# Kernel optimization log

Hardware: AMD Instinct MI355X
Metric: run time of the kernel (lower is better)

Reference implementation:

```python
import math
import jax, jax.numpy as jnp
import numpy as np

B, S, DIM = 1, 2048, 2048
N_HEADS, N_KV_HEADS = 32, 8
HEAD_DIM = DIM // N_HEADS  # 64
HIDDEN = 8192  # 4*dim, already a multiple of 256
EPS = 1e-5


def setup_inputs() -> dict:
    key = jax.random.key(0)
    ks = jax.random.split(key, 10)

    def xavier(k, shape):
        lim = math.sqrt(6.0 / (shape[0] + shape[1]))
        return jax.random.uniform(k, shape, jnp.float32, -lim, lim)

    x = jax.random.normal(ks[0], (B, S, DIM), jnp.float32)
    c = jax.random.normal(ks[1], (B, DIM), jnp.float32)
    x_mask = jnp.ones((B, S), dtype=bool)
    # RoPE angles (theta=10000), freqs_cis = exp(i * pos * inv_freq) -> cos/sin parts
    inv_freq = 1.0 / (10000.0 ** (jnp.arange(0, HEAD_DIM, 2, dtype=jnp.float32) / HEAD_DIM))
    ang = jnp.arange(S, dtype=jnp.float32)[:, None] * inv_freq[None, :]  # [S, HEAD_DIM//2]
    freqs_cos = jnp.broadcast_to(jnp.cos(ang)[None], (B, S, HEAD_DIM // 2))
    freqs_sin = jnp.broadcast_to(jnp.sin(ang)[None], (B, S, HEAD_DIM // 2))
    qkv_out = (N_HEADS + 2 * N_KV_HEADS) * HEAD_DIM
    return dict(
        x=x, x_mask=x_mask, freqs_cos=freqs_cos, freqs_sin=freqs_sin, c=c,
        w_qkv=xavier(ks[2], (qkv_out, DIM)),
        w_out=xavier(ks[3], (DIM, N_HEADS * HEAD_DIM)),
        q_norm_w=jnp.ones((HEAD_DIM,), jnp.float32),
        k_norm_w=jnp.ones((HEAD_DIM,), jnp.float32),
        attn_norm1_w=jnp.ones((DIM,), jnp.float32),
        attn_norm2_w=jnp.ones((DIM,), jnp.float32),
        ffn_norm1_w=jnp.ones((DIM,), jnp.float32),
        ffn_norm2_w=jnp.ones((DIM,), jnp.float32),
        w1=xavier(ks[4], (HIDDEN, DIM)),
        w2=xavier(ks[5], (DIM, HIDDEN)),
        w3=xavier(ks[6], (HIDDEN, DIM)),
        w_ada=0.02 * jax.random.normal(ks[7], (4 * DIM, DIM), jnp.float32),
        b_ada=jnp.zeros((4 * DIM,), jnp.float32),
    )


def rms_norm(x, w, eps=EPS):
    x32 = x.astype(jnp.float32)
    return (x32 * jax.lax.rsqrt(jnp.mean(x32 * x32, -1, keepdims=True) + eps)).astype(x.dtype) * w


def apply_rope(x, cos, sin):
    # x: [b,s,h,d]; complex pairing of consecutive elements (view_as_complex)
    xr, xi = x[..., 0::2], x[..., 1::2]
    c = cos[:, :, None, :]  # broadcast over heads (freqs_cis.unsqueeze(2))
    s = sin[:, :, None, :]
    return jnp.stack([xr * c - xi * s, xr * s + xi * c], axis=-1).reshape(x.shape)


def reference(x, x_mask, freqs_cos, freqs_sin, c, w_qkv, w_out, q_norm_w, k_norm_w,
              attn_norm1_w, attn_norm2_w, ffn_norm1_w, ffn_norm2_w, w1, w2, w3,
              w_ada, b_ada):
    b, s, _ = x.shape
    n_rep = N_HEADS // N_KV_HEADS
    # AdaLN modulation: SiLU -> Linear -> 4 chunks
    mod = jax.nn.silu(c) @ w_ada.T + b_ada                      # [b, 4*dim]
    scale_msa, gate_msa, scale_mlp, gate_mlp = jnp.split(mod, 4, axis=-1)
    # ---- attention branch ----
    h = rms_norm(x, attn_norm1_w) * (1.0 + scale_msa[:, None, :])
    qkv = h @ w_qkv.T
    q, k, v = jnp.split(qkv, [N_HEADS * HEAD_DIM, (N_HEADS + N_KV_HEADS) * HEAD_DIM], axis=-1)
    q = q.reshape(b, s, N_HEADS, HEAD_DIM)
    k = k.reshape(b, s, N_KV_HEADS, HEAD_DIM)
    v = v.reshape(b, s, N_KV_HEADS, HEAD_DIM)
    q = rms_norm(q, q_norm_w)
    k = rms_norm(k, k_norm_w)
    q = apply_rope(q, freqs_cos, freqs_sin)
    k = apply_rope(k, freqs_cos, freqs_sin)
    # GQA: repeat each kv head n_rep times consecutively (unsqueeze+repeat+flatten)
    k = jnp.repeat(k, n_rep, axis=2)
    v = jnp.repeat(v, n_rep, axis=2)
    scale = math.sqrt(1.0 / HEAD_DIM)
    scores = jnp.einsum('bqhd,bkhd->bhqk', q, k) * scale         # [b,H,s,s]
    scores = jnp.where(x_mask[:, None, None, :], scores, -1e30)
    probs = jax.nn.softmax(scores, axis=-1)
    attn = jnp.einsum('bhqk,bkhd->bqhd', probs, v).reshape(b, s, N_HEADS * HEAD_DIM)
    attn = attn @ w_out.T
    x = x + jnp.tanh(gate_msa)[:, None, :] * rms_norm(attn, attn_norm2_w)
    # ---- SwiGLU FFN branch ----
    h = rms_norm(x, ffn_norm1_w) * (1.0 + scale_mlp[:, None, :])
    ffn = (jax.nn.silu(h @ w1.T) * (h @ w3.T)) @ w2.T
    x = x + jnp.tanh(gate_mlp)[:, None, :] * rms_norm(ffn, ffn_norm2_w)
    return x
```

## Files before the change

### kernel.cpp

```cpp
#include <hip/hip_runtime.h>
#include <hip/hip_bf16.h>
#include <cstdint>

typedef __hip_bfloat16 bf16;
typedef __attribute__((ext_vector_type(8))) short s8v;
typedef __attribute__((ext_vector_type(4))) float f32x4;

#define MFMA_BF16(a,b,c) __builtin_amdgcn_mfma_f32_16x16x32_bf16((a),(b),(c),0,0,0)

__device__ __forceinline__ float bf2f(bf16 v) { return __bfloat162float(v); }
__device__ __forceinline__ bf16 f2bf(float v) { return __float2bfloat16(v); }
__device__ __forceinline__ short f2bfbits(float v) {
  bf16 b = __float2bfloat16(v);
  short s; __builtin_memcpy(&s, &b, 2); return s;
}
__device__ __forceinline__ void g2lds16(const void* g, void* l) {
  __builtin_amdgcn_global_load_lds((__attribute__((address_space(1))) void*)(g),
                                   (__attribute__((address_space(3))) void*)(l), 16, 0, 0);
}
__device__ __forceinline__ void load8(const bf16* p, float v[8]) {
  uint4 r = *reinterpret_cast<const uint4*>(p);
  v[0]=__uint_as_float(r.x<<16); v[1]=__uint_as_float(r.x&0xffff0000u);
  v[2]=__uint_as_float(r.y<<16); v[3]=__uint_as_float(r.y&0xffff0000u);
  v[4]=__uint_as_float(r.z<<16); v[5]=__uint_as_float(r.z&0xffff0000u);
  v[6]=__uint_as_float(r.w<<16); v[7]=__uint_as_float(r.w&0xffff0000u);
}
__device__ __forceinline__ void loadf8(const float* p, float v[8]) {
  float4 a = *(const float4*)p, b = *(const float4*)(p + 4);
  v[0]=a.x; v[1]=a.y; v[2]=a.z; v[3]=a.w;
  v[4]=b.x; v[5]=b.y; v[6]=b.z; v[7]=b.w;
}
__device__ __forceinline__ s8v cvt8(const float* p) {
  float4 a = *(const float4*)p, b = *(const float4*)(p + 4);
  s8v r;
  r[0]=f2bfbits(a.x); r[1]=f2bfbits(a.y); r[2]=f2bfbits(a.z); r[3]=f2bfbits(a.w);
  r[4]=f2bfbits(b.x); r[5]=f2bfbits(b.y); r[6]=f2bfbits(b.z); r[7]=f2bfbits(b.w);
  return r;
}

__global__ __launch_bounds__(256) void ndt_cvt(
    const float* __restrict__ s, bf16* __restrict__ d, long n) {
  long i = ((long)blockIdx.x * 256 + threadIdx.x) * 8;
  if (i >= n) return;
  *(s8v*)(d + i) = cvt8(s + i);
}

__global__ __launch_bounds__(256) void ndt_ada(
    const float* __restrict__ c, const float* __restrict__ w_ada,
    const float* __restrict__ b_ada, float* __restrict__ mods) {
  const int wave = threadIdx.x >> 6, lane = threadIdx.x & 63;
  const int out = blockIdx.x * 4 + wave;
  const float4* wrow = (const float4*)(w_ada + (long)out * 2048);
  const float4* c4 = (const float4*)c;
  float acc = 0.f;
  for (int k = lane; k < 512; k += 64) {
    float4 wv = wrow[k];
    float4 cv = c4[k];
    acc += (cv.x / (1.f + __expf(-cv.x))) * wv.x;
    acc += (cv.y / (1.f + __expf(-cv.y))) * wv.y;
    acc += (cv.z / (1.f + __expf(-cv.z))) * wv.z;
    acc += (cv.w / (1.f + __expf(-cv.w))) * wv.w;
  }
  #pragma unroll
  for (int o = 32; o; o >>= 1) acc += __shfl_xor(acc, o, 64);
  if (lane == 0) {
    float m = acc + b_ada[out];
    int grp = out >> 11, idx = out & 2047;
    mods[grp * 2048 + idx] = (grp & 1) ? tanhf(m) : (1.f + m);
  }
}

__global__ __launch_bounds__(256) void ndt_norm_mod(
    const float* __restrict__ x, const float* __restrict__ w,
    const float* __restrict__ smod, bf16* __restrict__ out) {
  const int t = blockIdx.x, tid = threadIdx.x;
  __shared__ float red[4];
  float v[8];
  loadf8(x + (long)t * 2048 + tid * 8, v);
  float ss = 0.f;
  #pragma unroll
  for (int i = 0; i < 8; i++) ss += v[i] * v[i];
  #pragma unroll
  for (int o = 32; o; o >>= 1) ss += __shfl_xor(ss, o, 64);
  if ((tid & 63) == 0) red[tid >> 6] = ss;
  __syncthreads();
  float r = rsqrtf((red[0]+red[1]+red[2]+red[3]) * (1.f/2048.f) + 1e-5f);
  #pragma unroll
  for (int i = 0; i < 8; i++) {
    int cc = tid * 8 + i;
    out[(long)t * 2048 + cc] = f2bf(v[i] * r * w[cc] * smod[cc]);
  }
}

template<int EPI>
__global__ __launch_bounds__(256) void ndt_gemm_bb(
    const bf16* __restrict__ A, const bf16* __restrict__ B,
    bf16* __restrict__ C, const bf16* __restrict__ aux,
    int M, int N, int K) {
  __shared__ alignas(16) short sA[128 * 32];
  __shared__ alignas(16) short sB[128 * 32];
  const int tid = threadIdx.x;
  const int wave = tid >> 6, lane = tid & 63;
  const int quad = lane >> 4, l15 = lane & 15;
  const int wm = (wave >> 1) << 6, wn = (wave & 1) << 6;
  const long m0 = (long)blockIdx.x * 128, n0 = (long)blockIdx.y * 128;
  f32x4 zero4 = {0.f, 0.f, 0.f, 0.f};
  f32x4 acc[4][4];
  #pragma unroll
  for (int i = 0; i < 4; i++)
    #pragma unroll
    for (int j = 0; j < 4; j++) acc[i][j] = zero4;
  const int srow = lane >> 2;
  const int skc  = (lane & 3) * 8;
  for (int k0 = 0; k0 < K; k0 += 32) {
    #pragma unroll
    for (int it = 0; it < 2; it++) {
      int seg = wave * 2 + it;
      int row = seg * 16 + srow;
      g2lds16(A + (m0 + row) * (long)K + k0 + skc, (char*)sA + seg * 1024);
      g2lds16(B + (n0 + row) * (long)K + k0 + skc, (char*)sB + seg * 1024);
    }
    __syncthreads();
    s8v af[4], bfr[4];
    #pragma unroll
    for (int i = 0; i < 4; i++) af[i]  = *(const s8v*)&sA[(wm + i*16 + l15)*32 + quad*8];
    #pragma unroll
    for (int j = 0; j < 4; j++) bfr[j] = *(const s8v*)&sB[(wn + j*16 + l15)*32 + quad*8];
    #pragma unroll
    for (int i = 0; i < 4; i++)
      #pragma unroll
      for (int j = 0; j < 4; j++)
        acc[i][j] = MFMA_BF16(af[i], bfr[j], acc[i][j]);
    __syncthreads();
  }
  #pragma unroll
  for (int i = 0; i < 4; i++) {
    long rg = m0 + wm + i*16 + quad*4;
    #pragma unroll
    for (int j = 0; j < 4; j++) {
      long cg = n0 + wn + j*16 + l15;
      #pragma unroll
      for (int r = 0; r < 4; r++) {
        float v = acc[i][j][r];
        long idx = (rg + r) * (long)N + cg;
        if (EPI == 1) v = v / (1.f + __expf(-v));
        if (EPI == 2) v = v * bf2f(aux[idx]);
        C[idx] = f2bf(v);
      }
    }
  }
}

template<int EPI>
__global__ __launch_bounds__(256) void ndt_gemm_bt(
    const bf16* __restrict__ A, const float* __restrict__ B,
    bf16* __restrict__ C, const bf16* __restrict__ aux,
    int M, int N, int K) {
  __shared__ alignas(16) short sA[128 * 32];
  __shared__ alignas(16) short sB[128 * 32];
  const int tid = threadIdx.x;
  const int wave = tid >> 6, lane = tid & 63;
  const int quad = lane >> 4, l15 = lane & 15;
  const int wm = (wave >> 1) << 6, wn = (wave & 1) << 6;
  const long m0 = (long)blockIdx.x * 128, n0 = (long)blockIdx.y * 128;
  f32x4 zero4 = {0.f, 0.f, 0.f, 0.f};
  f32x4 acc[4][4];
  #pragma unroll
  for (int i = 0; i < 4; i++)
    #pragma unroll
    for (int j = 0; j < 4; j++) acc[i][j] = zero4;
  const int srow = lane >> 2;
  const int skc  = (lane & 3) * 8;
  const int r0 = (wave * 2) * 16 + srow;
  const int r1 = (wave * 2 + 1) * 16 + srow;
  const bf16*  pa0 = A + (m0 + r0) * (long)K + skc;
  const bf16*  pa1 = A + (m0 + r1) * (long)K + skc;
  const float* pb0 = B + (n0 + r0) * (long)K + skc;
  const float* pb1 = B + (n0 + r1) * (long)K + skc;
  uint4* da0 = (uint4*)&sA[r0 * 32 + skc];
  uint4* da1 = (uint4*)&sA[r1 * 32 + skc];
  s8v* db0 = (s8v*)&sB[r0 * 32 + skc];
  s8v* db1 = (s8v*)&sB[r1 * 32 + skc];
  for (int k0 = 0; k0 < K; k0 += 32) {
    uint4 va0 = *(const uint4*)pa0; pa0 += 32;
    uint4 va1 = *(const uint4*)pa1; pa1 += 32;
    s8v vb0 = cvt8(pb0); pb0 += 32;
    s8v vb1 = cvt8(pb1); pb1 += 32;
    *da0 = va0; *da1 = va1; *db0 = vb0; *db1 = vb1;
    __syncthreads();
    s8v af[4], bfr[4];
    #pragma unroll
    for (int i = 0; i < 4; i++) af[i]  = *(const s8v*)&sA[(wm + i*16 + l15)*32 + quad*8];
    #pragma unroll
    for (int j = 0; j < 4; j++) bfr[j] = *(const s8v*)&sB[(wn + j*16 + l15)*32 + quad*8];
    #pragma unroll
    for (int i = 0; i < 4; i++)
      #pragma unroll
      for (int j = 0; j < 4; j++)
        acc[i][j] = MFMA_BF16(af[i], bfr[j], acc[i][j]);
    __syncthreads();
  }
  #pragma unroll
  for (int i = 0; i < 4; i++) {
    long rg = m0 + wm + i*16 + quad*4;
    #pragma unroll
    for (int j = 0; j < 4; j++) {
      long cg = n0 + wn + j*16 + l15;
      #pragma unroll
      for (int r = 0; r < 4; r++) {
        float v = acc[i][j][r];
        long idx = (rg + r) * (long)N + cg;
        if (EPI == 1) v = v / (1.f + __expf(-v));
        if (EPI == 2) v = v * bf2f(aux[idx]);
        C[idx] = f2bf(v);
      }
    }
  }
}

__global__ __launch_bounds__(256) void ndt_qkrope(
    const bf16* __restrict__ qkv, const float* __restrict__ qw, const float* __restrict__ kw,
    const float* __restrict__ fc, const float* __restrict__ fs,
    bf16* __restrict__ qb, bf16* __restrict__ kb, bf16* __restrict__ vb) {
  const int wid = blockIdx.x * 4 + (threadIdx.x >> 6);
  const int lane = threadIdx.x & 63;
  const int t = wid / 48;
  const int u = wid - t * 48;
  if (u < 40) {
    const bool isq = (u < 32);
    const int hh = isq ? u : (u - 32);
    const long src = (long)t * 3072 + (isq ? hh * 64 : 2048 + hh * 64) + lane;
    float v = bf2f(qkv[src]);
    float ss = v * v;
    #pragma unroll
    for (int o = 32; o; o >>= 1) ss += __shfl_xor(ss, o, 64);
    float r = rsqrtf(ss * (1.f/64.f) + 1e-5f);
    float y = v * r * (isq ? qw[lane] : kw[lane]);
    int j = lane >> 1;
    float cv = fc[t * 32 + j];
    float sv = fs[t * 32 + j];
    float p = __shfl_xor(y, 1, 64);
    float out = (lane & 1) ? (p * sv + y * cv) : (y * cv - p * sv);
    if (isq) qb[(long)t * 2048 + hh * 64 + lane] = f2bf(out);
    else     kb[(long)t * 512 + hh * 64 + lane] = f2bf(out);
  } else {
    const int vh = u - 40;
    vb[(long)t * 512 + vh * 64 + lane] = qkv[(long)t * 3072 + 2560 + vh * 64 + lane];
  }
}

__global__ __launch_bounds__(256) void ndt_attn(
    const bf16* __restrict__ qb, const bf16* __restrict__ kb,
    const bf16* __restrict__ vb, bf16* __restrict__ ob) {
  const int h = blockIdx.y;
  const int qblk = blockIdx.x;
  const int tid = threadIdx.x;
  const int wave = tid >> 6, lane = tid & 63;
  const int quad = lane >> 4, l15 = lane & 15;
  const int kh = h >> 2;
  __shared__ alignas(16) short kT[64 * 72];
  __shared__ alignas(16) short vT[64 * 72];
  __shared__ alignas(16) short pT[4][16 * 72];
  const int qrow = qblk * 64 + wave * 16 + l15;
  const short* qptr = (const short*)qb + (long)qrow * 2048 + h * 64;
  s8v qf0 = *(const s8v*)(qptr + quad * 8);
  s8v qf1 = *(const s8v*)(qptr + 32 + quad * 8);
  f32x4 zero4 = {0.f, 0.f, 0.f, 0.f};
  f32x4 o[4];
  float mr[4], lr[4];
  #pragma unroll
  for (int r = 0; r < 4; r++) { o[r] = zero4; mr[r] = -1e30f; lr[r] = 0.f; }
  const int skey = tid >> 2;
  const int sdg = (tid & 3) * 16;
  for (int kt = 0; kt < 32; kt++) {
    {
      const short* ksrc = (const short*)kb + ((long)(kt * 64 + skey) * 8 + kh) * 64 + sdg;
      *(uint4*)&kT[skey * 72 + sdg]     = *(const uint4*)(ksrc);
      *(uint4*)&kT[skey * 72 + sdg + 8] = *(const uint4*)(ksrc + 8);
      const short* vsrc = (const short*)vb + ((long)(kt * 64 + skey) * 8 + kh) * 64 + sdg;
      short tv[16];
      *(uint4*)&tv[0] = *(const uint4*)(vsrc);
      *(uint4*)&tv[8] = *(const uint4*)(vsrc + 8);
      #pragma unroll
      for (int i = 0; i < 16; i++) vT[(sdg + i) * 72 + skey] = tv[i];
    }
    __syncthreads();
    f32x4 s[4];
    #pragma unroll
    for (int b4 = 0; b4 < 4; b4++) {
      const short* kr = &kT[(b4 * 16 + l15) * 72];
      s8v kf0 = *(const s8v*)(kr + quad * 8);
      s8v kf1 = *(const s8v*)(kr + 32 + quad * 8);
      f32x4 z = zero4;
      z = MFMA_BF16(qf0, kf0, z);
      z = MFMA_BF16(qf1, kf1, z);
      s[b4] = z;
    }
    #pragma unroll
    for (int r = 0; r < 4; r++) {
      float mx = -1e30f;
      #pragma unroll
      for (int b4 = 0; b4 < 4; b4++) { float sv2 = s[b4][r] * 0.125f; s[b4][r] = sv2; mx = fmaxf(mx, sv2); }
      mx = fmaxf(mx, __shfl_xor(mx, 1, 64));
      mx = fmaxf(mx, __shfl_xor(mx, 2, 64));
      mx = fmaxf(mx, __shfl_xor(mx, 4, 64));
      mx = fmaxf(mx, __shfl_xor(mx, 8, 64));
      float nm = fmaxf(mr[r], mx);
      float alpha = __expf(mr[r] - nm);
      mr[r] = nm;
      float rs = 0.f;
      #pragma unroll
      for (int b4 = 0; b4 < 4; b4++) { float p = __expf(s[b4][r] - nm); s[b4][r] = p; rs += p; }
      rs += __shfl_xor(rs, 1, 64);
      rs += __shfl_xor(rs, 2, 64);
      rs += __shfl_xor(rs, 4, 64);
      rs += __shfl_xor(rs, 8, 64);
      lr[r] = lr[r] * alpha + rs;
      #pragma unroll
      for (int cb = 0; cb < 4; cb++) o[cb][r] *= alpha;
    }
    short* pw = &pT[wave][0];
    #pragma unroll
    for (int b4 = 0; b4 < 4; b4++)
      #pragma unroll
      for (int r = 0; r < 4; r++)
        pw[(quad * 4 + r) * 72 + b4 * 16 + l15] = f2bfbits(s[b4][r]);
    const short* pr = &pT[wave][0];
    s8v pf0 = *(const s8v*)(pr + l15 * 72 + quad * 8);
    s8v pf1 = *(const s8v*)(pr + l15 * 72 + 32 + quad * 8);
    #pragma unroll
    for (int cb = 0; cb < 4; cb++) {
      const short* vr = &vT[(cb * 16 + l15) * 72];
      s8v vf0 = *(const s8v*)(vr + quad * 8);
      s8v vf1 = *(const s8v*)(vr + 32 + quad * 8);
      o[cb] = MFMA_BF16(pf0, vf0, o[cb]);
      o[cb] = MFMA_BF16(pf1, vf1, o[cb]);
    }
    __syncthreads();
  }
  #pragma unroll
  for (int cb = 0; cb < 4; cb++)
    #pragma unroll
    for (int r = 0; r < 4; r++) {
      int tok = qblk * 64 + wave * 16 + quad * 4 + r;
      ob[(long)tok * 2048 + h * 64 + cb * 16 + l15] = f2bf(o[cb][r] / lr[r]);
    }
}

__global__ __launch_bounds__(256) void ndt_resid1(
    const float* __restrict__ x, const bf16* __restrict__ ao,
    const float* __restrict__ mods, const float* __restrict__ w_n2,
    const float* __restrict__ w_f1, float* __restrict__ x1, bf16* __restrict__ h2) {
  const int t = blockIdx.x, tid = threadIdx.x;
  __shared__ float red1[4], red2[4];
  const long base = (long)t * 2048;
  float a[8], xv[8], y[8];
  load8(ao + base + tid * 8, a);
  loadf8(x + base + tid * 8, xv);
  float ss = 0.f;
  #pragma unroll
  for (int i = 0; i < 8; i++) ss += a[i] * a[i];
  #pragma unroll
  for (int o = 32; o; o >>= 1) ss += __shfl_xor(ss, o, 64);
  if ((tid & 63) == 0) red1[tid >> 6] = ss;
  __syncthreads();
  float r1 = rsqrtf((red1[0]+red1[1]+red1[2]+red1[3]) * (1.f/2048.f) + 1e-5f);
  float ss2 = 0.f;
  #pragma unroll
  for (int i = 0; i < 8; i++) {
    int cc = tid * 8 + i;
    float yy = xv[i] + mods[2048 + cc] * (a[i] * r1 * w_n2[cc]);
    y[i] = yy; ss2 += yy * yy;
    x1[base + cc] = yy;
  }
  #pragma unroll
  for (int o = 32; o; o >>= 1) ss2 += __shfl_xor(ss2, o, 64);
  if ((tid & 63) == 0) red2[tid >> 6] = ss2;
  __syncthreads();
  float r2 = rsqrtf((red2[0]+red2[1]+red2[2]+red2[3]) * (1.f/2048.f) + 1e-5f);
  #pragma unroll
  for (int i = 0; i < 8; i++) {
    int cc = tid * 8 + i;
    h2[base + cc] = f2bf(y[i] * r2 * w_f1[cc] * mods[4096 + cc]);
  }
}

__global__ __launch_bounds__(256) void ndt_resid2(
    const float* __restrict__ x1, const bf16* __restrict__ ffn,
    const float* __restrict__ mods, const float* __restrict__ w_f2,
    float* __restrict__ out) {
  const int t = blockIdx.x, tid = threadIdx.x;
  __shared__ float red[4];
  const long base = (long)t * 2048;
  float f[8], xv[8];
  load8(ffn + base + tid * 8, f);
  loadf8(x1 + base + tid * 8, xv);
  float ss = 0.f;
  #pragma unroll
  for (int i = 0; i < 8; i++) ss += f[i] * f[i];
  #pragma unroll
  for (int o = 32; o; o >>= 1) ss += __shfl_xor(ss, o, 64);
  if ((tid & 63) == 0) red[tid >> 6] = ss;
  __syncthreads();
  float r = rsqrtf((red[0]+red[1]+red[2]+red[3]) * (1.f/2048.f) + 1e-5f);
  #pragma unroll
  for (int i = 0; i < 8; i++) {
    int cc = tid * 8 + i;
    out[base + cc] = xv[i] + mods[6144 + cc] * (f[i] * r * w_f2[cc]);
  }
}

extern "C" void kernel_launch(void* const* d_in, const int* in_sizes, int n_in,
                              void* d_out, int out_size, void* d_ws, size_t ws_size,
                              hipStream_t stream) {
  const float* x     = (const float*)d_in[0];
  const float* fc    = (const float*)d_in[2];
  const float* fs    = (const float*)d_in[3];
  const float* c     = (const float*)d_in[4];
  const float* w_qkv = (const float*)d_in[5];
  const float* w_out = (const float*)d_in[6];
  const float* q_nw  = (const float*)d_in[7];
  const float* k_nw  = (const float*)d_in[8];
  const float* an1   = (const float*)d_in[9];
  const float* an2   = (const float*)d_in[10];
  const float* fn1   = (const float*)d_in[11];
  const float* fn2   = (const float*)d_in[12];
  const float* w1    = (const float*)d_in[13];
  const float* w2    = (const float*)d_in[14];
  const float* w3    = (const float*)d_in[15];
  const float* w_ada = (const float*)d_in[16];
  const float* b_ada = (const float*)d_in[17];
  float* out = (float*)d_out;

  const size_t MB = 1024 * 1024;
  char* w = (char*)d_ws;
  float* mods = (float*)(w);
  char* base = w + 32768;
  bf16* h1   = (bf16*)(base);
  bf16* attn = h1;
  bf16* ffn  = h1;
  bf16* qkv  = (bf16*)(base + 8 * MB);
  bf16* ao   = qkv;
  bf16* qb   = (bf16*)(base + 20 * MB);
  bf16* h2   = qb;
  bf16* kb   = (bf16*)(base + 28 * MB);
  bf16* vb   = (bf16*)(base + 30 * MB);
  float* x1  = (float*)(base + 32 * MB);
  bf16* t1   = (bf16*)(base + 48 * MB);
  bf16* Wa   = (bf16*)(base + 80 * MB);
  bf16* Wb   = (bf16*)(base + 112 * MB);
  const size_t needed = 32768 + 144 * MB;

  ndt_ada<<<2048, 256, 0, stream>>>(c, w_ada, b_ada, mods);
  ndt_norm_mod<<<2048, 256, 0, stream>>>(x, an1, mods, h1);

  if (ws_size >= needed) {
    ndt_cvt<<<3072, 256, 0, stream>>>(w_qkv, Wa, 6291456L);
    ndt_gemm_bb<0><<<dim3(16, 24), 256, 0, stream>>>(h1, Wa, qkv, nullptr, 2048, 3072, 2048);
    ndt_qkrope<<<24576, 256, 0, stream>>>(qkv, q_nw, k_nw, fc, fs, qb, kb, vb);
    ndt_attn<<<dim3(32, 32), 256, 0, stream>>>(qb, kb, vb, attn);
    ndt_cvt<<<2048, 256, 0, stream>>>(w_out, Wa, 4194304L);
    ndt_gemm_bb<0><<<dim3(16, 16), 256, 0, stream>>>(attn, Wa, ao, nullptr, 2048, 2048, 2048);
    ndt_resid1<<<2048, 256, 0, stream>>>(x, ao, mods, an2, fn1, x1, h2);
    ndt_cvt<<<8192, 256, 0, stream>>>(w1, Wa, 16777216L);
    ndt_cvt<<<8192, 256, 0, stream>>>(w3, Wb, 16777216L);
    ndt_gemm_bb<1><<<dim3(16, 64), 256, 0, stream>>>(h2, Wa, t1, nullptr, 2048, 8192, 2048);
    ndt_gemm_bb<2><<<dim3(16, 64), 256, 0, stream>>>(h2, Wb, t1, t1, 2048, 8192, 2048);
    ndt_cvt<<<8192, 256, 0, stream>>>(w2, Wa, 16777216L);
    ndt_gemm_bb<0><<<dim3(16, 16), 256, 0, stream>>>(t1, Wa, ffn, nullptr, 2048, 2048, 8192);
  } else {
    ndt_gemm_bt<0><<<dim3(16, 24), 256, 0, stream>>>(h1, w_qkv, qkv, nullptr, 2048, 3072, 2048);
    ndt_qkrope<<<24576, 256, 0, stream>>>(qkv, q_nw, k_nw, fc, fs, qb, kb, vb);
    ndt_attn<<<dim3(32, 32), 256, 0, stream>>>(qb, kb, vb, attn);
    ndt_gemm_bt<0><<<dim3(16, 16), 256, 0, stream>>>(attn, w_out, ao, nullptr, 2048, 2048, 2048);
    ndt_resid1<<<2048, 256, 0, stream>>>(x, ao, mods, an2, fn1, x1, h2);
    ndt_gemm_bt<1><<<dim3(16, 64), 256, 0, stream>>>(h2, w1, t1, nullptr, 2048, 8192, 2048);
    ndt_gemm_bt<2><<<dim3(16, 64), 256, 0, stream>>>(h2, w3, t1, t1, 2048, 8192, 2048);
    ndt_gemm_bt<0><<<dim3(16, 16), 256, 0, stream>>>(t1, w2, ffn, nullptr, 2048, 2048, 8192);
  }
  ndt_resid2<<<2048, 256, 0, stream>>>(x1, ffn, mods, fn2, out);
}
```

Baseline: 971.1 us.

## Add 256x256 double-buffered 8-wave GEMM for FFN up/gate projections

Adds a new GEMM kernel with 256x256 output tiles, 512 threads (8 waves) and a double-buffered LDS pipeline. It interleaves direct global-to-LDS loads with MFMA phases separated by barriers, uses an XOR swizzle against LDS bank conflicts, raises wave priority around the MFMA bursts, and remaps workgroups across XCDs. It replaces the 128x128 GEMM only for the w1 and w3 projections, aiming for more data reuse and better load/compute overlap. The cost is 128KB of LDS per block and a large accumulator register footprint, which limits occupancy.

```diff
diff --git a/kernel.cpp b/kernel.cpp
--- a/kernel.cpp
+++ b/kernel.cpp
@@ -142,6 +142,147 @@
       #pragma unroll
       for (int r = 0; r < 4; r++) {
         float v = acc[i][j][r];
+        long idx = (rg + r) * (long)N + cg;
+        if (EPI == 1) v = v / (1.f + __expf(-v));
+        if (EPI == 2) v = v * bf2f(aux[idx]);
+        C[idx] = f2bf(v);
+      }
+    }
+  }
+}
+
+__device__ __forceinline__ void stage64(const bf16* __restrict__ G, long g0,
+                                        int K, int t, char* tile, int q, int tid) {
+  int L = q * 8192 + tid * 16;
+  int Ls = L ^ (((L >> 9) & 1) << 5);
+  const char* src = (const char*)(G + (g0 + (Ls >> 7)) * (long)K + t * 64) + (Ls & 127);
+  g2lds16(src, tile + L);
+}
+
+__device__ __forceinline__ void phase_bar() {
+  asm volatile("" ::: "memory");
+  __builtin_amdgcn_s_barrier();
+  asm volatile("" ::: "memory");
+}
+
+#define READ_A8(tA, h) do { \
+  _Pragma("unroll") for (int i_ = 0; i_ < 4; i_++) { \
+    int row_ = wm * 128 + (h) * 64 + i_ * 16 + l15; \
+    _Pragma("unroll") for (int kk_ = 0; kk_ < 2; kk_++) { \
+      int P_ = row_ * 128 + kk_ * 64 + quad * 16; \
+      af[kk_][i_] = *(const s8v*)((tA) + (P_ ^ (((P_ >> 9) & 1) << 5))); } } } while (0)
+
+#define READ_B8(tB, nh, bfreg) do { \
+  _Pragma("unroll") for (int j_ = 0; j_ < 2; j_++) { \
+    int col_ = wn * 64 + (nh) * 32 + j_ * 16 + l15; \
+    _Pragma("unroll") for (int kk_ = 0; kk_ < 2; kk_++) { \
+      int P_ = col_ * 128 + kk_ * 64 + quad * 16; \
+      bfreg[kk_][j_] = *(const s8v*)((tB) + (P_ ^ (((P_ >> 9) & 1) << 5))); } } } while (0)
+
+#define MMQ8(h, nh, bfreg) do { \
+  __builtin_amdgcn_s_setprio(1); \
+  _Pragma("unroll") for (int i_ = 0; i_ < 4; i_++) \
+    _Pragma("unroll") for (int j_ = 0; j_ < 2; j_++) { \
+      acc[(h)*4 + i_][(nh)*2 + j_] = MFMA_BF16(af[0][i_], bfreg[0][j_], acc[(h)*4 + i_][(nh)*2 + j_]); \
+      acc[(h)*4 + i_][(nh)*2 + j_] = MFMA_BF16(af[1][i_], bfreg[1][j_], acc[(h)*4 + i_][(nh)*2 + j_]); } \
+  __builtin_amdgcn_s_setprio(0); } while (0)
+
+template<int EPI>
+__global__ __launch_bounds__(512, 2) void ndt_gemm8(
+    const bf16* __restrict__ A, const bf16* __restrict__ B,
+    bf16* __restrict__ C, const bf16* __restrict__ aux,
+    int M, int N, int K) {
+  __shared__ alignas(16) short lds8[65536];
+  char* const tA0 = (char*)lds8;
+  char* const tB0 = tA0 + 32768;
+  char* const tA1 = tA0 + 65536;
+  char* const tB1 = tA0 + 98304;
+
+  const int tid = threadIdx.x;
+  const int wid = tid >> 6, lane = tid & 63;
+  const int quad = lane >> 4, l15 = lane & 15;
+  const int wm = wid >> 2, wn = wid & 3;
+
+  const int nbx = gridDim.x;
+  int bid = blockIdx.y * nbx + blockIdx.x;
+  const int nwg = nbx * (int)gridDim.y;
+  if ((nwg & 7) == 0) bid = (bid & 7) * (nwg >> 3) + (bid >> 3);
+  const long m0 = (long)(bid % nbx) * 256;
+  const long n0 = (long)(bid / nbx) * 256;
+
+  const int NT = K >> 6;
+  const int NI = NT >> 1;
+
+  f32x4 acc[8][4];
+  f32x4 zero4 = {0.f, 0.f, 0.f, 0.f};
+  #pragma unroll
+  for (int i = 0; i < 8; i++)
+    #pragma unroll
+    for (int j = 0; j < 4; j++) acc[i][j] = zero4;
+
+  s8v af[2][4], bf0[2][2], bf1[2][2];
+
+  #pragma unroll
+  for (int q = 0; q < 4; q++) stage64(A, m0, K, 0, tA0, q, tid);
+  #pragma unroll
+  for (int q = 0; q < 4; q++) stage64(B, n0, K, 0, tB0, q, tid);
+  #pragma unroll
+  for (int q = 0; q < 4; q++) stage64(A, m0, K, 1, tA1, q, tid);
+  stage64(B, n0, K, 1, tB1, 0, tid);
+  stage64(B, n0, K, 1, tB1, 1, tid);
+  asm volatile("s_waitcnt vmcnt(6)" ::: "memory");
+  phase_bar();
+
+  for (int it = 0; it < NI; ++it) {
+    const int T = 2 * it;
+    const int t2 = (T + 2 < NT) ? T + 2 : NT - 1;
+    const int t3 = (T + 3 < NT) ? T + 3 : NT - 1;
+    READ_A8(tA0, 0);
+    READ_B8(tB0, 0, bf0);
+    stage64(B, n0, K, T + 1, tB1, 2, tid);
+    stage64(B, n0, K, T + 1, tB1, 3, tid);
+    phase_bar(); MMQ8(0, 0, bf0); phase_bar();
+    READ_B8(tB0, 1, bf1);
+    stage64(A, m0, K, t2, tA0, 0, tid);
+    stage64(A, m0, K, t2, tA0, 2, tid);
+    phase_bar(); MMQ8(0, 1, bf1); phase_bar();
+    READ_A8(tA0, 1);
+    stage64(B, n0, K, t2, tB0, 0, tid);
+    stage64(B, n0, K, t2, tB0, 1, tid);
+    phase_bar(); MMQ8(1, 0, bf0); phase_bar();
+    stage64(A, m0, K, t2, tA0, 1, tid);
+    stage64(A, m0, K, t2, tA0, 3, tid);
+    asm volatile("s_waitcnt vmcnt(6)" ::: "memory");
+    phase_bar(); MMQ8(1, 1, bf1); phase_bar();
+    READ_A8(tA1, 0);
+    READ_B8(tB1, 0, bf0);
+    stage64(B, n0, K, t2, tB0, 2, tid);
+    stage64(B, n0, K, t2, tB0, 3, tid);
+    phase_bar(); MMQ8(0, 0, bf0); phase_bar();
+    READ_B8(tB1, 1, bf1);
+    stage64(A, m0, K, t3, tA1, 0, tid);
+    stage64(A, m0, K, t3, tA1, 2, tid);
+    phase_bar(); MMQ8(0, 1, bf1); phase_bar();
+    READ_A8(tA1, 1);
+    stage64(B, n0, K, t3, tB1, 0, tid);
+    stage64(B, n0, K, t3, tB1, 1, tid);
+    phase_bar(); MMQ8(1, 0, bf0); phase_bar();
+    stage64(A, m0, K, t3, tA1, 1, tid);
+    stage64(A, m0, K, t3, tA1, 3, tid);
+    asm volatile("s_waitcnt vmcnt(6)" ::: "memory");
+    phase_bar(); MMQ8(1, 1, bf1); phase_bar();
+  }
+  asm volatile("s_waitcnt vmcnt(0)" ::: "memory");
+
+  #pragma unroll
+  for (int mi = 0; mi < 8; mi++) {
+    long rg = m0 + wm * 128 + mi * 16 + quad * 4;
+    #pragma unroll
+    for (int nj = 0; nj < 4; nj++) {
+      long cg = n0 + wn * 64 + nj * 16 + l15;
+      #pragma unroll
+      for (int r = 0; r < 4; r++) {
+        float v = acc[mi][nj][r];
         long idx = (rg + r) * (long)N + cg;
         if (EPI == 1) v = v / (1.f + __expf(-v));
         if (EPI == 2) v = v * bf2f(aux[idx]);
@@ -464,8 +605,8 @@
     ndt_resid1<<<2048, 256, 0, stream>>>(x, ao, mods, an2, fn1, x1, h2);
     ndt_cvt<<<8192, 256, 0, stream>>>(w1, Wa, 16777216L);
     ndt_cvt<<<8192, 256, 0, stream>>>(w3, Wb, 16777216L);
-    ndt_gemm_bb<1><<<dim3(16, 64), 256, 0, stream>>>(h2, Wa, t1, nullptr, 2048, 8192, 2048);
-    ndt_gemm_bb<2><<<dim3(16, 64), 256, 0, stream>>>(h2, Wb, t1, t1, 2048, 8192, 2048);
+    ndt_gemm8<1><<<dim3(8, 32), 512, 0, stream>>>(h2, Wa, t1, nullptr, 2048, 8192, 2048);
+    ndt_gemm8<2><<<dim3(8, 32), 512, 0, stream>>>(h2, Wb, t1, t1, 2048, 8192, 2048);
     ndt_cvt<<<8192, 256, 0, stream>>>(w2, Wa, 16777216L);
     ndt_gemm_bb<0><<<dim3(16, 16), 256, 0, stream>>>(t1, Wa, ffn, nullptr, 2048, 2048, 8192);
   } else {
```

Result: faster. 893.1 us (-8.0%).
